# Kernel optimization log

Measured on AMD Instinct MI355X. Metric: run time of the kernel, lower is better.

The kernel has to match this reference:

```python
import jax, jax.numpy as jnp
import numpy as np

MARGIN = 0.4
ALPHA = 0.01


def _pairwise_dist(emb):
    sq = jnp.sum(emb * emb, axis=1)
    d2 = jnp.maximum(sq[:, None] + sq[None, :] - 2.0 * (emb @ emb.T), 0.0)
    safe = jnp.where(d2 > 0, d2, 1.0)
    return jnp.where(d2 > 0, jnp.sqrt(safe), 0.0)


def setup_inputs() -> dict:
    key = jax.random.key(0)
    ka, kp, kn = jax.random.split(key, 3)
    B, D = 4096, 128
    return {
        "a": jax.random.normal(ka, (B, D), dtype=jnp.float32),
        "p": jax.random.normal(kp, (B, D), dtype=jnp.float32),
        "n": jax.random.normal(kn, (B, D), dtype=jnp.float32),
    }


def reference(a, p, n):
    B = a.shape[0]
    emb = jnp.concatenate([a, p, n], axis=0)            # [3B, D]
    labels = jnp.tile(jnp.arange(B), 3)                 # [3B]
    dist = _pairwise_dist(emb)                          # [3B, 3B]
    same = labels[:, None] == labels[None, :]           # exactly 3 True per row (incl. diag)
    # Every row has >=2 positives (3 incl. self) and >=1 negative, so all rows count.
    pos_max = jnp.max(jnp.where(same, dist, -jnp.inf), axis=1)
    neg_min = jnp.min(jnp.where(same, jnp.inf, dist), axis=1)
    loss = jnp.mean(jnp.maximum(pos_max - neg_min + MARGIN, 0.0))
    reg = jnp.mean((jnp.abs(emb) - 1.0) ** 2)
    return loss + ALPHA * reg
```

## Files before the change

kernel.cpp:

```cpp
#include <hip/hip_runtime.h>

#define NROWS 12288
#define BSZ   4096
#define DIM   128
#define NB    48
#define NTILES (NB * (NB + 1) / 2)
#define COLS_PER_BLOCK 256
#define NSTRIPS (COLS_PER_BLOCK / 32)

typedef __bf16 bf16x8 __attribute__((ext_vector_type(8)));
typedef float  f32x4  __attribute__((ext_vector_type(4)));

__device__ __forceinline__ unsigned short f2bf(float f) {
  unsigned int u = __float_as_uint(f);
  u = u + 0x7FFFu + ((u >> 16) & 1u);
  return (unsigned short)(u >> 16);
}
__device__ __forceinline__ float bf2f(unsigned short h) {
  return __uint_as_float(((unsigned int)h) << 16);
}

__global__ void prep_k(const float* __restrict__ a, const float* __restrict__ p,
                       const float* __restrict__ nn,
                       unsigned short* __restrict__ embh, float* __restrict__ sq,
                       unsigned int* __restrict__ negbits,
                       float* __restrict__ posmax2, float* __restrict__ regpart) {
  const int w = threadIdx.x >> 6, lane = threadIdx.x & 63;
  const int i = blockIdx.x * 4 + w;
  const float2 av = reinterpret_cast<const float2*>(a  + (size_t)i * DIM)[lane];
  const float2 pv = reinterpret_cast<const float2*>(p  + (size_t)i * DIM)[lane];
  const float2 nv = reinterpret_cast<const float2*>(nn + (size_t)i * DIM)[lane];

  const unsigned short ha0 = f2bf(av.x), ha1 = f2bf(av.y);
  const unsigned short hp0 = f2bf(pv.x), hp1 = f2bf(pv.y);
  const unsigned short hn0 = f2bf(nv.x), hn1 = f2bf(nv.y);
  reinterpret_cast<ushort2*>(embh + (size_t)i * DIM)[lane]             = make_ushort2(ha0, ha1);
  reinterpret_cast<ushort2*>(embh + (size_t)(BSZ + i) * DIM)[lane]     = make_ushort2(hp0, hp1);
  reinterpret_cast<ushort2*>(embh + (size_t)(2 * BSZ + i) * DIM)[lane] = make_ushort2(hn0, hn1);

  float rax = bf2f(ha0), ray = bf2f(ha1);
  float rpx = bf2f(hp0), rpy = bf2f(hp1);
  float rnx = bf2f(hn0), rny = bf2f(hn1);
  float sa = rax * rax + ray * ray;
  float sp = rpx * rpx + rpy * rpy;
  float sn = rnx * rnx + rny * rny;

  float t0 = fabsf(av.x) - 1.f, t1 = fabsf(av.y) - 1.f;
  float t2 = fabsf(pv.x) - 1.f, t3 = fabsf(pv.y) - 1.f;
  float t4 = fabsf(nv.x) - 1.f, t5 = fabsf(nv.y) - 1.f;
  float rg = t0 * t0 + t1 * t1 + t2 * t2 + t3 * t3 + t4 * t4 + t5 * t5;

  float dx, dy;
  dx = av.x - pv.x; dy = av.y - pv.y; float dap = dx * dx + dy * dy;
  dx = av.x - nv.x; dy = av.y - nv.y; float dan = dx * dx + dy * dy;
  dx = pv.x - nv.x; dy = pv.y - nv.y; float dpn = dx * dx + dy * dy;

  for (int m = 32; m; m >>= 1) {
    sa  += __shfl_xor(sa, m);  sp  += __shfl_xor(sp, m);  sn  += __shfl_xor(sn, m);
    rg  += __shfl_xor(rg, m);
    dap += __shfl_xor(dap, m); dan += __shfl_xor(dan, m); dpn += __shfl_xor(dpn, m);
  }
  if (lane == 0) {
    sq[i] = sa; sq[BSZ + i] = sp; sq[2 * BSZ + i] = sn;
    negbits[i] = negbits[BSZ + i] = negbits[2 * BSZ + i] = 0x7F800000u;
    posmax2[i]           = fmaxf(dap, dan);
    posmax2[BSZ + i]     = fmaxf(dap, dpn);
    posmax2[2 * BSZ + i] = fmaxf(dan, dpn);
    regpart[i] = rg;
  }
}

__global__ __launch_bounds__(256, 3) void negmin_k(
    const unsigned short* __restrict__ embh,
    const float* __restrict__ sq,
    unsigned int* __restrict__ negbits) {
  __shared__ __align__(16) char ldsB[2][8192];
  __shared__ float cminw[4][COLS_PER_BLOCK];
  const int tid  = threadIdx.x;
  const int w    = tid >> 6;
  const int lane = tid & 63;
  const int c16  = lane & 15;
  const int q    = lane >> 4;

  int rem = blockIdx.x, ti = 0;
  while (rem >= NB - ti) { rem -= NB - ti; ++ti; }
  const int tj   = ti + rem;
  const bool diag = (ti == tj);
  const int wRow    = ti * 256 + w * 64;
  const int colBase = tj * 256;
  const int rot     = blockIdx.x & (NSTRIPS - 1);

  bf16x8 afrag[4][4];
  {
    const char* abase = (const char*)embh + (size_t)(wRow + c16) * 256 + q * 16;
#pragma unroll
    for (int mt = 0; mt < 4; ++mt)
#pragma unroll
      for (int ks = 0; ks < 4; ++ks)
        afrag[mt][ks] = *reinterpret_cast<const bf16x8*>(abase + mt * 4096 + ks * 64);
  }

  float sqrow[4][4];
  {
    const int rbase = wRow + q * 4;
#pragma unroll
    for (int mt = 0; mt < 4; ++mt) {
      const f32x4 t = *reinterpret_cast<const f32x4*>(&sq[rbase + mt * 16]);
#pragma unroll
      for (int r = 0; r < 4; ++r) sqrow[mt][r] = t[r];
    }
  }

  float minv[4][4];
#pragma unroll
  for (int mt = 0; mt < 4; ++mt)
#pragma unroll
    for (int r = 0; r < 4; ++r) minv[mt][r] = __builtin_inff();

  auto stage = [&](int sidx, int b) {
#pragma unroll
    for (int h = 0; h < 2; ++h) {
      const int kc = w * 2 + h;
      const char* gp = (const char*)embh +
          (size_t)(colBase + sidx * 32 + (kc & 1) * 16 + c16) * 256 +
          (kc >> 1) * 64 + q * 16;
      __builtin_amdgcn_global_load_lds(
          (const __attribute__((address_space(1))) unsigned int*)gp,
          (__attribute__((address_space(3))) unsigned int*)(&ldsB[b][kc * 1024]),
          16, 0, 0);
    }
  };

  int strip = rot;
  stage(strip, 0);
  __syncthreads();
  {
    int s1 = strip + 1; if (s1 >= NSTRIPS) s1 -= NSTRIPS;
    stage(s1, 1);
  }

  for (int c = 0; c < NSTRIPS; ++c) {
    const int b = c & 1;
    const int colStart = colBase + strip * 32;
    const float sq0 = sq[colStart + c16];
    const float sq1 = sq[colStart + 16 + c16];

    f32x4 acc[4][2] = {};
#pragma unroll
    for (int ks = 0; ks < 4; ++ks)
#pragma unroll
      for (int ct = 0; ct < 2; ++ct) {
        const bf16x8 bfr =
            *reinterpret_cast<const bf16x8*>(&ldsB[b][(ks * 2 + ct) * 1024 + lane * 16]);
#pragma unroll
        for (int mt = 0; mt < 4; ++mt)
          acc[mt][ct] =
              __builtin_amdgcn_mfma_f32_16x16x32_bf16(afrag[mt][ks], bfr, acc[mt][ct], 0, 0, 0);
      }

    __syncthreads();
    if (c + 2 < NSTRIPS) {
      int s2 = strip + 2; if (s2 >= NSTRIPS) s2 -= NSTRIPS;
      stage(s2, b);
    }

    const int dd = (colStart - wRow) & 4095;
    float cf0 = __builtin_inff(), cf1 = __builtin_inff();
    if (dd < 76 || dd > 4064) {
#pragma unroll
      for (int mt = 0; mt < 4; ++mt)
#pragma unroll
        for (int ct = 0; ct < 2; ++ct) {
          const float sqb = ct ? sq1 : sq0;
          const int lvc = dd + ct * 16 + c16 - q * 4;
#pragma unroll
          for (int r = 0; r < 4; ++r) {
            float e = fmaf(-2.f, acc[mt][ct][r], sqb) + sqrow[mt][r];
            const int K = mt * 16 + r;
            if (lvc == K || lvc == K + 4096) e = __builtin_inff();
            minv[mt][r] = fminf(minv[mt][r], e);
            if (ct) cf1 = fminf(cf1, e); else cf0 = fminf(cf0, e);
          }
        }
    } else {
#pragma unroll
      for (int mt = 0; mt < 4; ++mt)
#pragma unroll
        for (int ct = 0; ct < 2; ++ct) {
          const float sqb = ct ? sq1 : sq0;
#pragma unroll
          for (int r = 0; r < 4; ++r) {
            float e = fmaf(-2.f, acc[mt][ct][r], sqb) + sqrow[mt][r];
            minv[mt][r] = fminf(minv[mt][r], e);
            if (ct) cf1 = fminf(cf1, e); else cf0 = fminf(cf0, e);
          }
        }
    }

    if (!diag) {
      cf0 = fminf(cf0, __shfl_xor(cf0, 16));
      cf0 = fminf(cf0, __shfl_xor(cf0, 32));
      cf1 = fminf(cf1, __shfl_xor(cf1, 16));
      cf1 = fminf(cf1, __shfl_xor(cf1, 32));
      if (q == 0) {
        cminw[w][strip * 32 + c16]      = cf0;
        cminw[w][strip * 32 + 16 + c16] = cf1;
      }
    }

    strip = strip + 1; if (strip >= NSTRIPS) strip -= NSTRIPS;
  }

#pragma unroll
  for (int mt = 0; mt < 4; ++mt)
#pragma unroll
    for (int r = 0; r < 4; ++r) {
      float v = minv[mt][r];
      v = fminf(v, __shfl_xor(v, 1));
      v = fminf(v, __shfl_xor(v, 2));
      v = fminf(v, __shfl_xor(v, 4));
      v = fminf(v, __shfl_xor(v, 8));
      if (c16 == 0) {
        const int row = wRow + mt * 16 + q * 4 + r;
        atomicMin(&negbits[row], __float_as_uint(fmaxf(v, 0.f)));
      }
    }

  __syncthreads();
  if (!diag) {
    const float m = fminf(fminf(cminw[0][tid], cminw[1][tid]),
                          fminf(cminw[2][tid], cminw[3][tid]));
    atomicMin(&negbits[colBase + tid], __float_as_uint(fmaxf(m, 0.f)));
  }
}

__global__ void final_k(const float* __restrict__ posmax2,
                        const unsigned int* __restrict__ negbits,
                        const float* __restrict__ regpart, float* __restrict__ out) {
  __shared__ float red[16], redr[16];
  const int tid = threadIdx.x;
  float s = 0.f;
  for (int i = tid; i < NROWS; i += 1024) {
    const float pm = sqrtf(posmax2[i]);
    const float nm = sqrtf(__uint_as_float(negbits[i]));
    s += fmaxf(pm - nm + 0.4f, 0.f);
  }
  float rg = 0.f;
  for (int i = tid; i < BSZ; i += 1024) rg += regpart[i];
  for (int m = 32; m; m >>= 1) { s += __shfl_xor(s, m); rg += __shfl_xor(rg, m); }
  if ((tid & 63) == 0) { red[tid >> 6] = s; redr[tid >> 6] = rg; }
  __syncthreads();
  if (tid == 0) {
    float t = 0.f, tr = 0.f;
#pragma unroll
    for (int k = 0; k < 16; ++k) { t += red[k]; tr += redr[k]; }
    out[0] = t / (float)NROWS + 0.01f * (tr / (float)(NROWS * DIM));
  }
}

extern "C" void kernel_launch(void* const* d_in, const int* in_sizes, int n_in,
                              void* d_out, int out_size, void* d_ws, size_t ws_size,
                              hipStream_t stream) {
  const float* a  = (const float*)d_in[0];
  const float* p  = (const float*)d_in[1];
  const float* nn = (const float*)d_in[2];
  float* out = (float*)d_out;
  char* ws = (char*)d_ws;

  const size_t EMBH_BYTES = (size_t)NROWS * DIM * 2;
  unsigned short* embh    = (unsigned short*)ws;
  float*          sq      = (float*)(ws + EMBH_BYTES);
  unsigned int*   negbit  = (unsigned int*)(ws + EMBH_BYTES + (size_t)NROWS * 4);
  float*          pos2    = (float*)(ws + EMBH_BYTES + (size_t)NROWS * 8);
  float*          regpart = (float*)(ws + EMBH_BYTES + (size_t)NROWS * 12);

  prep_k<<<BSZ / 4, 256, 0, stream>>>(a, p, nn, embh, sq, negbit, pos2, regpart);
  negmin_k<<<dim3(NTILES), 256, 0, stream>>>(embh, sq, negbit);
  final_k<<<1, 1024, 0, stream>>>(pos2, negbit, regpart, out);
}
```

Baseline: 108.7 us.

## Fuse final reduction into negmin via last-block counter and stage 64-column chunks

Removes the separate final_k launch. Each negmin tile block bumps a global counter, and the last block to finish does the loss and regularisation reduction, reading negbits through atomics. The counter is zeroed in prep_k. The LDS staging buffer is also doubled so each pipeline step loads 64 columns, not 32. That halves the number of barrier and stage iterations, at the cost of more shared memory per block and a serial tail reduction run by one 256-thread block.

```diff
diff --git a/kernel.cpp b/kernel.cpp
--- a/kernel.cpp
+++ b/kernel.cpp
@@ -6,7 +6,7 @@
 #define NB    48
 #define NTILES (NB * (NB + 1) / 2)
 #define COLS_PER_BLOCK 256
-#define NSTRIPS (COLS_PER_BLOCK / 32)
+#define NPAIR 4
 
 typedef __bf16 bf16x8 __attribute__((ext_vector_type(8)));
 typedef float  f32x4  __attribute__((ext_vector_type(4)));
@@ -24,7 +24,9 @@
                        const float* __restrict__ nn,
                        unsigned short* __restrict__ embh, float* __restrict__ sq,
                        unsigned int* __restrict__ negbits,
-                       float* __restrict__ posmax2, float* __restrict__ regpart) {
+                       float* __restrict__ posmax2, float* __restrict__ regpart,
+                       unsigned int* __restrict__ tilecnt) {
+  if (blockIdx.x == 0 && threadIdx.x == 0) *tilecnt = 0u;
   const int w = threadIdx.x >> 6, lane = threadIdx.x & 63;
   const int i = blockIdx.x * 4 + w;
   const float2 av = reinterpret_cast<const float2*>(a  + (size_t)i * DIM)[lane];
@@ -73,9 +75,15 @@
 __global__ __launch_bounds__(256, 3) void negmin_k(
     const unsigned short* __restrict__ embh,
     const float* __restrict__ sq,
-    unsigned int* __restrict__ negbits) {
-  __shared__ __align__(16) char ldsB[2][8192];
+    unsigned int* __restrict__ negbits,
+    const float* __restrict__ posmax2,
+    const float* __restrict__ regpart,
+    unsigned int* __restrict__ tilecnt,
+    float* __restrict__ out) {
+  __shared__ __align__(16) char ldsB[2][16384];
   __shared__ float cminw[4][COLS_PER_BLOCK];
+  __shared__ float redf[4], redr[4];
+  __shared__ unsigned int sdone;
   const int tid  = threadIdx.x;
   const int w    = tid >> 6;
   const int lane = tid & 63;
@@ -88,7 +96,7 @@
   const bool diag = (ti == tj);
   const int wRow    = ti * 256 + w * 64;
   const int colBase = tj * 256;
-  const int rot     = blockIdx.x & (NSTRIPS - 1);
+  const int rot     = blockIdx.x & (NPAIR - 1);
 
   bf16x8 afrag[4][4];
   {
@@ -117,98 +125,97 @@
 #pragma unroll
     for (int r = 0; r < 4; ++r) minv[mt][r] = __builtin_inff();
 
-  auto stage = [&](int sidx, int b) {
-#pragma unroll
-    for (int h = 0; h < 2; ++h) {
-      const int kc = w * 2 + h;
+  auto stage = [&](int sidx_, int b_) {
+#pragma unroll
+    for (int h = 0; h < 4; ++h) {
+      const int kc = w * 4 + h;
       const char* gp = (const char*)embh +
-          (size_t)(colBase + sidx * 32 + (kc & 1) * 16 + c16) * 256 +
-          (kc >> 1) * 64 + q * 16;
+          (size_t)(colBase + sidx_ * 64 + (kc >> 3) * 32 + (kc & 1) * 16 + c16) * 256 +
+          ((kc >> 1) & 3) * 64 + q * 16;
       __builtin_amdgcn_global_load_lds(
           (const __attribute__((address_space(1))) unsigned int*)gp,
-          (__attribute__((address_space(3))) unsigned int*)(&ldsB[b][kc * 1024]),
+          (__attribute__((address_space(3))) unsigned int*)(&ldsB[b_][kc * 1024]),
           16, 0, 0);
     }
   };
 
-  int strip = rot;
-  stage(strip, 0);
+  int sidx = rot;
+  stage(sidx, 0);
   __syncthreads();
-  {
-    int s1 = strip + 1; if (s1 >= NSTRIPS) s1 -= NSTRIPS;
-    stage(s1, 1);
-  }
-
-  for (int c = 0; c < NSTRIPS; ++c) {
+  stage((sidx + 1) & (NPAIR - 1), 1);
+
+  for (int c = 0; c < NPAIR; ++c) {
     const int b = c & 1;
-    const int colStart = colBase + strip * 32;
-    const float sq0 = sq[colStart + c16];
-    const float sq1 = sq[colStart + 16 + c16];
-
-    f32x4 acc[4][2] = {};
-#pragma unroll
-    for (int ks = 0; ks < 4; ++ks)
-#pragma unroll
-      for (int ct = 0; ct < 2; ++ct) {
-        const bf16x8 bfr =
-            *reinterpret_cast<const bf16x8*>(&ldsB[b][(ks * 2 + ct) * 1024 + lane * 16]);
+    const int colS0 = colBase + sidx * 64;
+
+#pragma unroll
+    for (int ss = 0; ss < 2; ++ss) {
+      const int colStart = colS0 + ss * 32;
+      const float sq0 = sq[colStart + c16];
+      const float sq1 = sq[colStart + 16 + c16];
+
+      f32x4 acc[4][2] = {};
+#pragma unroll
+      for (int ks = 0; ks < 4; ++ks)
+#pragma unroll
+        for (int ct = 0; ct < 2; ++ct) {
+          const bf16x8 bfr = *reinterpret_cast<const bf16x8*>(
+              &ldsB[b][(ss * 8 + ks * 2 + ct) * 1024 + lane * 16]);
+#pragma unroll
+          for (int mt = 0; mt < 4; ++mt)
+            acc[mt][ct] = __builtin_amdgcn_mfma_f32_16x16x32_bf16(
+                afrag[mt][ks], bfr, acc[mt][ct], 0, 0, 0);
+        }
+
+      const int dd = (colStart - wRow) & 4095;
+      float cf0 = __builtin_inff(), cf1 = __builtin_inff();
+      if (dd < 76 || dd > 4064) {
 #pragma unroll
         for (int mt = 0; mt < 4; ++mt)
-          acc[mt][ct] =
-              __builtin_amdgcn_mfma_f32_16x16x32_bf16(afrag[mt][ks], bfr, acc[mt][ct], 0, 0, 0);
-      }
+#pragma unroll
+          for (int ct = 0; ct < 2; ++ct) {
+            const float sqb = ct ? sq1 : sq0;
+            const int lvc = dd + ct * 16 + c16 - q * 4;
+#pragma unroll
+            for (int r = 0; r < 4; ++r) {
+              float e = fmaf(-2.f, acc[mt][ct][r], sqb) + sqrow[mt][r];
+              const int K = mt * 16 + r;
+              if (lvc == K || lvc == K + 4096) e = __builtin_inff();
+              minv[mt][r] = fminf(minv[mt][r], e);
+              if (ct) cf1 = fminf(cf1, e); else cf0 = fminf(cf0, e);
+            }
+          }
+      } else {
+#pragma unroll
+        for (int mt = 0; mt < 4; ++mt)
+#pragma unroll
+          for (int ct = 0; ct < 2; ++ct) {
+            const float sqb = ct ? sq1 : sq0;
+#pragma unroll
+            for (int r = 0; r < 4; ++r) {
+              float e = fmaf(-2.f, acc[mt][ct][r], sqb) + sqrow[mt][r];
+              minv[mt][r] = fminf(minv[mt][r], e);
+              if (ct) cf1 = fminf(cf1, e); else cf0 = fminf(cf0, e);
+            }
+          }
+      }
+
+      if (!diag) {
+        cf0 = fminf(cf0, __shfl_xor(cf0, 16));
+        cf0 = fminf(cf0, __shfl_xor(cf0, 32));
+        cf1 = fminf(cf1, __shfl_xor(cf1, 16));
+        cf1 = fminf(cf1, __shfl_xor(cf1, 32));
+        if (q == 0) {
+          cminw[w][sidx * 64 + ss * 32 + c16]      = cf0;
+          cminw[w][sidx * 64 + ss * 32 + 16 + c16] = cf1;
+        }
+      }
+    }
 
     __syncthreads();
-    if (c + 2 < NSTRIPS) {
-      int s2 = strip + 2; if (s2 >= NSTRIPS) s2 -= NSTRIPS;
-      stage(s2, b);
-    }
-
-    const int dd = (colStart - wRow) & 4095;
-    float cf0 = __builtin_inff(), cf1 = __builtin_inff();
-    if (dd < 76 || dd > 4064) {
-#pragma unroll
-      for (int mt = 0; mt < 4; ++mt)
-#pragma unroll
-        for (int ct = 0; ct < 2; ++ct) {
-          const float sqb = ct ? sq1 : sq0;
-          const int lvc = dd + ct * 16 + c16 - q * 4;
-#pragma unroll
-          for (int r = 0; r < 4; ++r) {
-            float e = fmaf(-2.f, acc[mt][ct][r], sqb) + sqrow[mt][r];
-            const int K = mt * 16 + r;
-            if (lvc == K || lvc == K + 4096) e = __builtin_inff();
-            minv[mt][r] = fminf(minv[mt][r], e);
-            if (ct) cf1 = fminf(cf1, e); else cf0 = fminf(cf0, e);
-          }
-        }
-    } else {
-#pragma unroll
-      for (int mt = 0; mt < 4; ++mt)
-#pragma unroll
-        for (int ct = 0; ct < 2; ++ct) {
-          const float sqb = ct ? sq1 : sq0;
-#pragma unroll
-          for (int r = 0; r < 4; ++r) {
-            float e = fmaf(-2.f, acc[mt][ct][r], sqb) + sqrow[mt][r];
-            minv[mt][r] = fminf(minv[mt][r], e);
-            if (ct) cf1 = fminf(cf1, e); else cf0 = fminf(cf0, e);
-          }
-        }
-    }
-
-    if (!diag) {
-      cf0 = fminf(cf0, __shfl_xor(cf0, 16));
-      cf0 = fminf(cf0, __shfl_xor(cf0, 32));
-      cf1 = fminf(cf1, __shfl_xor(cf1, 16));
-      cf1 = fminf(cf1, __shfl_xor(cf1, 32));
-      if (q == 0) {
-        cminw[w][strip * 32 + c16]      = cf0;
-        cminw[w][strip * 32 + 16 + c16] = cf1;
-      }
-    }
-
-    strip = strip + 1; if (strip >= NSTRIPS) strip -= NSTRIPS;
+    if (c + 2 < NPAIR) stage((sidx + 2) & (NPAIR - 1), b);
+
+    sidx = (sidx + 1) & (NPAIR - 1);
   }
 
 #pragma unroll
@@ -232,29 +239,44 @@
                           fminf(cminw[2][tid], cminw[3][tid]));
     atomicMin(&negbits[colBase + tid], __float_as_uint(fmaxf(m, 0.f)));
   }
-}
-
-__global__ void final_k(const float* __restrict__ posmax2,
-                        const unsigned int* __restrict__ negbits,
-                        const float* __restrict__ regpart, float* __restrict__ out) {
-  __shared__ float red[16], redr[16];
-  const int tid = threadIdx.x;
-  float s = 0.f;
-  for (int i = tid; i < NROWS; i += 1024) {
-    const float pm = sqrtf(posmax2[i]);
-    const float nm = sqrtf(__uint_as_float(negbits[i]));
-    s += fmaxf(pm - nm + 0.4f, 0.f);
-  }
-  float rg = 0.f;
-  for (int i = tid; i < BSZ; i += 1024) rg += regpart[i];
-  for (int m = 32; m; m >>= 1) { s += __shfl_xor(s, m); rg += __shfl_xor(rg, m); }
-  if ((tid & 63) == 0) { red[tid >> 6] = s; redr[tid >> 6] = rg; }
+
+  __threadfence();
+  if (tid == 0) sdone = atomicAdd(tilecnt, 1u);
   __syncthreads();
-  if (tid == 0) {
-    float t = 0.f, tr = 0.f;
-#pragma unroll
-    for (int k = 0; k < 16; ++k) { t += red[k]; tr += redr[k]; }
-    out[0] = t / (float)NROWS + 0.01f * (tr / (float)(NROWS * DIM));
+  if (sdone == NTILES - 1) {
+    __threadfence();
+    float s = 0.f;
+    for (int i0 = tid; i0 < NROWS; i0 += 1024) {
+      float t0, t1, t2, t3;
+      {
+        const int i = i0;
+        t0 = fmaxf(sqrtf(posmax2[i]) - sqrtf(__uint_as_float(atomicOr(&negbits[i], 0u))) + 0.4f, 0.f);
+      }
+      {
+        const int i = i0 + 256;
+        t1 = fmaxf(sqrtf(posmax2[i]) - sqrtf(__uint_as_float(atomicOr(&negbits[i], 0u))) + 0.4f, 0.f);
+      }
+      {
+        const int i = i0 + 512;
+        t2 = fmaxf(sqrtf(posmax2[i]) - sqrtf(__uint_as_float(atomicOr(&negbits[i], 0u))) + 0.4f, 0.f);
+      }
+      {
+        const int i = i0 + 768;
+        t3 = fmaxf(sqrtf(posmax2[i]) - sqrtf(__uint_as_float(atomicOr(&negbits[i], 0u))) + 0.4f, 0.f);
+      }
+      s += t0; s += t1; s += t2; s += t3;
+    }
+    float rg = 0.f;
+    for (int i = tid; i < BSZ; i += 256) rg += regpart[i];
+    for (int m = 32; m; m >>= 1) { s += __shfl_xor(s, m); rg += __shfl_xor(rg, m); }
+    if (lane == 0) { redf[w] = s; redr[w] = rg; }
+    __syncthreads();
+    if (tid == 0) {
+      float t = 0.f, tr = 0.f;
+#pragma unroll
+      for (int k = 0; k < 4; ++k) { t += redf[k]; tr += redr[k]; }
+      out[0] = t / (float)NROWS + 0.01f * (tr / (float)(NROWS * DIM));
+    }
   }
 }
 
@@ -273,8 +295,8 @@
   unsigned int*   negbit  = (unsigned int*)(ws + EMBH_BYTES + (size_t)NROWS * 4);
   float*          pos2    = (float*)(ws + EMBH_BYTES + (size_t)NROWS * 8);
   float*          regpart = (float*)(ws + EMBH_BYTES + (size_t)NROWS * 12);
-
-  prep_k<<<BSZ / 4, 256, 0, stream>>>(a, p, nn, embh, sq, negbit, pos2, regpart);
-  negmin_k<<<dim3(NTILES), 256, 0, stream>>>(embh, sq, negbit);
-  final_k<<<1, 1024, 0, stream>>>(pos2, negbit, regpart, out);
-}
+  unsigned int*   tilecnt = (unsigned int*)(ws + EMBH_BYTES + (size_t)NROWS * 16);
+
+  prep_k<<<BSZ / 4, 256, 0, stream>>>(a, p, nn, embh, sq, negbit, pos2, regpart, tilecnt);
+  negmin_k<<<dim3(NTILES), 256, 0, stream>>>(embh, sq, negbit, pos2, regpart, tilecnt, out);
+}
```

Measured after the change: 191.5 us. 1.76x slower.

## Stage two column strips per barrier and fully unroll strip loop

Applied to the files above, without the earlier changes.

The negmin kernel now loads two 32-column strips (64 columns) into each LDS buffer, doubling the LDS staging footprint, and processes them between barriers. This halves the number of __syncthreads and staging rounds. The per-block rotation of the starting strip is removed, and column squared norms are preloaded into registers up front. The larger LDS footprint and the fully unrolled loop raise LDS and register pressure, which may reduce occupancy under launch_bounds(256,3). Dropping the rotation may also increase contention between blocks reading the same columns.

```diff
diff --git a/kernel.cpp b/kernel.cpp
--- a/kernel.cpp
+++ b/kernel.cpp
@@ -6,7 +6,7 @@
 #define NB    48
 #define NTILES (NB * (NB + 1) / 2)
 #define COLS_PER_BLOCK 256
-#define NSTRIPS (COLS_PER_BLOCK / 32)
+#define NPAIR 4
 
 typedef __bf16 bf16x8 __attribute__((ext_vector_type(8)));
 typedef float  f32x4  __attribute__((ext_vector_type(4)));
@@ -74,7 +74,7 @@
     const unsigned short* __restrict__ embh,
     const float* __restrict__ sq,
     unsigned int* __restrict__ negbits) {
-  __shared__ __align__(16) char ldsB[2][8192];
+  __shared__ __align__(16) char ldsB[2][16384];
   __shared__ float cminw[4][COLS_PER_BLOCK];
   const int tid  = threadIdx.x;
   const int w    = tid >> 6;
@@ -88,7 +88,6 @@
   const bool diag = (ti == tj);
   const int wRow    = ti * 256 + w * 64;
   const int colBase = tj * 256;
-  const int rot     = blockIdx.x & (NSTRIPS - 1);
 
   bf16x8 afrag[4][4];
   {
@@ -111,104 +110,108 @@
     }
   }
 
+  float sqc[8][2];
+#pragma unroll
+  for (int s = 0; s < 8; ++s) {
+    sqc[s][0] = sq[colBase + s * 32 + c16];
+    sqc[s][1] = sq[colBase + s * 32 + 16 + c16];
+  }
+
   float minv[4][4];
 #pragma unroll
   for (int mt = 0; mt < 4; ++mt)
 #pragma unroll
     for (int r = 0; r < 4; ++r) minv[mt][r] = __builtin_inff();
 
-  auto stage = [&](int sidx, int b) {
-#pragma unroll
-    for (int h = 0; h < 2; ++h) {
-      const int kc = w * 2 + h;
+  auto stage = [&](int sidx_, int b_) {
+#pragma unroll
+    for (int h = 0; h < 4; ++h) {
+      const int kc = w * 4 + h;
       const char* gp = (const char*)embh +
-          (size_t)(colBase + sidx * 32 + (kc & 1) * 16 + c16) * 256 +
-          (kc >> 1) * 64 + q * 16;
+          (size_t)(colBase + sidx_ * 64 + (kc >> 3) * 32 + (kc & 1) * 16 + c16) * 256 +
+          ((kc >> 1) & 3) * 64 + q * 16;
       __builtin_amdgcn_global_load_lds(
           (const __attribute__((address_space(1))) unsigned int*)gp,
-          (__attribute__((address_space(3))) unsigned int*)(&ldsB[b][kc * 1024]),
+          (__attribute__((address_space(3))) unsigned int*)(&ldsB[b_][kc * 1024]),
           16, 0, 0);
     }
   };
 
-  int strip = rot;
-  stage(strip, 0);
+  stage(0, 0);
   __syncthreads();
-  {
-    int s1 = strip + 1; if (s1 >= NSTRIPS) s1 -= NSTRIPS;
-    stage(s1, 1);
-  }
-
-  for (int c = 0; c < NSTRIPS; ++c) {
+  stage(1, 1);
+
+#pragma unroll
+  for (int c = 0; c < NPAIR; ++c) {
     const int b = c & 1;
-    const int colStart = colBase + strip * 32;
-    const float sq0 = sq[colStart + c16];
-    const float sq1 = sq[colStart + 16 + c16];
-
-    f32x4 acc[4][2] = {};
-#pragma unroll
-    for (int ks = 0; ks < 4; ++ks)
-#pragma unroll
-      for (int ct = 0; ct < 2; ++ct) {
-        const bf16x8 bfr =
-            *reinterpret_cast<const bf16x8*>(&ldsB[b][(ks * 2 + ct) * 1024 + lane * 16]);
+
+#pragma unroll
+    for (int ss = 0; ss < 2; ++ss) {
+      const int sAbs = c * 2 + ss;
+      const int colStart = colBase + sAbs * 32;
+      const float sq0 = sqc[sAbs][0];
+      const float sq1 = sqc[sAbs][1];
+
+      f32x4 acc[4][2] = {};
+#pragma unroll
+      for (int ks = 0; ks < 4; ++ks)
+#pragma unroll
+        for (int ct = 0; ct < 2; ++ct) {
+          const bf16x8 bfr = *reinterpret_cast<const bf16x8*>(
+              &ldsB[b][(ss * 8 + ks * 2 + ct) * 1024 + lane * 16]);
+#pragma unroll
+          for (int mt = 0; mt < 4; ++mt)
+            acc[mt][ct] = __builtin_amdgcn_mfma_f32_16x16x32_bf16(
+                afrag[mt][ks], bfr, acc[mt][ct], 0, 0, 0);
+        }
+
+      const int dd = (colStart - wRow) & 4095;
+      float cf0 = __builtin_inff(), cf1 = __builtin_inff();
+      if (dd < 76 || dd > 4064) {
 #pragma unroll
         for (int mt = 0; mt < 4; ++mt)
-          acc[mt][ct] =
-              __builtin_amdgcn_mfma_f32_16x16x32_bf16(afrag[mt][ks], bfr, acc[mt][ct], 0, 0, 0);
+#pragma unroll
+          for (int ct = 0; ct < 2; ++ct) {
+            const float sqb = ct ? sq1 : sq0;
+            const int lvc = dd + ct * 16 + c16 - q * 4;
+#pragma unroll
+            for (int r = 0; r < 4; ++r) {
+              float e = fmaf(-2.f, acc[mt][ct][r], sqb) + sqrow[mt][r];
+              const int K = mt * 16 + r;
+              if (lvc == K || lvc == K + 4096) e = __builtin_inff();
+              minv[mt][r] = fminf(minv[mt][r], e);
+              if (ct) cf1 = fminf(cf1, e); else cf0 = fminf(cf0, e);
+            }
+          }
+      } else {
+#pragma unroll
+        for (int mt = 0; mt < 4; ++mt)
+#pragma unroll
+          for (int ct = 0; ct < 2; ++ct) {
+            const float sqb = ct ? sq1 : sq0;
+#pragma unroll
+            for (int r = 0; r < 4; ++r) {
+              float e = fmaf(-2.f, acc[mt][ct][r], sqb) + sqrow[mt][r];
+              minv[mt][r] = fminf(minv[mt][r], e);
+              if (ct) cf1 = fminf(cf1, e); else cf0 = fminf(cf0, e);
+            }
+          }
       }
 
+      if (!diag) {
+        cf0 = fminf(cf0, __shfl_xor(cf0, 16));
+        cf0 = fminf(cf0, __shfl_xor(cf0, 32));
+        cf1 = fminf(cf1, __shfl_xor(cf1, 16));
+        cf1 = fminf(cf1, __shfl_xor(cf1, 32));
+        if (q == 0) {
+          cminw[w][sAbs * 32 + c16]      = cf0;
+          cminw[w][sAbs * 32 + 16 + c16] = cf1;
+        }
+      }
+    }
+
     __syncthreads();
-    if (c + 2 < NSTRIPS) {
-      int s2 = strip + 2; if (s2 >= NSTRIPS) s2 -= NSTRIPS;
-      stage(s2, b);
-    }
-
-    const int dd = (colStart - wRow) & 4095;
-    float cf0 = __builtin_inff(), cf1 = __builtin_inff();
-    if (dd < 76 || dd > 4064) {
-#pragma unroll
-      for (int mt = 0; mt < 4; ++mt)
-#pragma unroll
-        for (int ct = 0; ct < 2; ++ct) {
-          const float sqb = ct ? sq1 : sq0;
-          const int lvc = dd + ct * 16 + c16 - q * 4;
-#pragma unroll
-          for (int r = 0; r < 4; ++r) {
-            float e = fmaf(-2.f, acc[mt][ct][r], sqb) + sqrow[mt][r];
-            const int K = mt * 16 + r;
-            if (lvc == K || lvc == K + 4096) e = __builtin_inff();
-            minv[mt][r] = fminf(minv[mt][r], e);
-            if (ct) cf1 = fminf(cf1, e); else cf0 = fminf(cf0, e);
-          }
-        }
-    } else {
-#pragma unroll
-      for (int mt = 0; mt < 4; ++mt)
-#pragma unroll
-        for (int ct = 0; ct < 2; ++ct) {
-          const float sqb = ct ? sq1 : sq0;
-#pragma unroll
-          for (int r = 0; r < 4; ++r) {
-            float e = fmaf(-2.f, acc[mt][ct][r], sqb) + sqrow[mt][r];
-            minv[mt][r] = fminf(minv[mt][r], e);
-            if (ct) cf1 = fminf(cf1, e); else cf0 = fminf(cf0, e);
-          }
-        }
-    }
-
-    if (!diag) {
-      cf0 = fminf(cf0, __shfl_xor(cf0, 16));
-      cf0 = fminf(cf0, __shfl_xor(cf0, 32));
-      cf1 = fminf(cf1, __shfl_xor(cf1, 16));
-      cf1 = fminf(cf1, __shfl_xor(cf1, 32));
-      if (q == 0) {
-        cminw[w][strip * 32 + c16]      = cf0;
-        cminw[w][strip * 32 + 16 + c16] = cf1;
-      }
-    }
-
-    strip = strip + 1; if (strip >= NSTRIPS) strip -= NSTRIPS;
+    if (c + 2 < NPAIR) stage(c + 2, b);
   }
 
 #pragma unroll
```

Result: slower. 124.6 us (+14.7%).

## Stage four column strips per batch instead of double-buffered strip pipeline

Applied to the files above, without the earlier changes.

Replaces the rotating double-buffered strip loop with two phases. Each phase loads four strips into a four-slot LDS buffer, synchronizes once, then computes all four strips. This cuts the number of block-wide barriers and drops the per-block strip rotation. In exchange, LDS use doubles to 32 KB, loads no longer overlap with compute inside a phase, and all blocks now start on the same strip.

```diff
diff --git a/kernel.cpp b/kernel.cpp
--- a/kernel.cpp
+++ b/kernel.cpp
@@ -74,7 +74,7 @@
     const unsigned short* __restrict__ embh,
     const float* __restrict__ sq,
     unsigned int* __restrict__ negbits) {
-  __shared__ __align__(16) char ldsB[2][8192];
+  __shared__ __align__(16) char ldsB[4][8192];
   __shared__ float cminw[4][COLS_PER_BLOCK];
   const int tid  = threadIdx.x;
   const int w    = tid >> 6;
@@ -88,7 +88,6 @@
   const bool diag = (ti == tj);
   const int wRow    = ti * 256 + w * 64;
   const int colBase = tj * 256;
-  const int rot     = blockIdx.x & (NSTRIPS - 1);
 
   bf16x8 afrag[4][4];
   {
@@ -105,9 +104,9 @@
     const int rbase = wRow + q * 4;
 #pragma unroll
     for (int mt = 0; mt < 4; ++mt) {
-      const f32x4 t = *reinterpret_cast<const f32x4*>(&sq[rbase + mt * 16]);
-#pragma unroll
-      for (int r = 0; r < 4; ++r) sqrow[mt][r] = t[r];
+      const f32x4 tv = *reinterpret_cast<const f32x4*>(&sq[rbase + mt * 16]);
+#pragma unroll
+      for (int r = 0; r < 4; ++r) sqrow[mt][r] = tv[r];
     }
   }
 
@@ -131,17 +130,8 @@
     }
   };
 
-  int strip = rot;
-  stage(strip, 0);
-  __syncthreads();
-  {
-    int s1 = strip + 1; if (s1 >= NSTRIPS) s1 -= NSTRIPS;
-    stage(s1, 1);
-  }
-
-  for (int c = 0; c < NSTRIPS; ++c) {
-    const int b = c & 1;
-    const int colStart = colBase + strip * 32;
+  auto computeStrip = [&](int sAbs, int slot) {
+    const int colStart = colBase + sAbs * 32;
     const float sq0 = sq[colStart + c16];
     const float sq1 = sq[colStart + 16 + c16];
 
@@ -151,18 +141,12 @@
 #pragma unroll
       for (int ct = 0; ct < 2; ++ct) {
         const bf16x8 bfr =
-            *reinterpret_cast<const bf16x8*>(&ldsB[b][(ks * 2 + ct) * 1024 + lane * 16]);
+            *reinterpret_cast<const bf16x8*>(&ldsB[slot][(ks * 2 + ct) * 1024 + lane * 16]);
 #pragma unroll
         for (int mt = 0; mt < 4; ++mt)
           acc[mt][ct] =
               __builtin_amdgcn_mfma_f32_16x16x32_bf16(afrag[mt][ks], bfr, acc[mt][ct], 0, 0, 0);
       }
-
-    __syncthreads();
-    if (c + 2 < NSTRIPS) {
-      int s2 = strip + 2; if (s2 >= NSTRIPS) s2 -= NSTRIPS;
-      stage(s2, b);
-    }
 
     const int dd = (colStart - wRow) & 4095;
     float cf0 = __builtin_inff(), cf1 = __builtin_inff();
@@ -203,13 +187,24 @@
       cf1 = fminf(cf1, __shfl_xor(cf1, 16));
       cf1 = fminf(cf1, __shfl_xor(cf1, 32));
       if (q == 0) {
-        cminw[w][strip * 32 + c16]      = cf0;
-        cminw[w][strip * 32 + 16 + c16] = cf1;
+        cminw[w][sAbs * 32 + c16]      = cf0;
+        cminw[w][sAbs * 32 + 16 + c16] = cf1;
       }
     }
-
-    strip = strip + 1; if (strip >= NSTRIPS) strip -= NSTRIPS;
-  }
+  };
+
+#pragma unroll
+  for (int s = 0; s < 4; ++s) stage(s, s);
+  __syncthreads();
+#pragma unroll
+  for (int s = 0; s < 4; ++s) computeStrip(s, s);
+
+  __syncthreads();
+#pragma unroll
+  for (int s = 4; s < 8; ++s) stage(s, s - 4);
+  __syncthreads();
+#pragma unroll
+  for (int s = 4; s < 8; ++s) computeStrip(s, s - 4);
 
 #pragma unroll
   for (int mt = 0; mt < 4; ++mt)
```

Result: slower. 119.6 us (+10.0%).
